# Kernel optimization log

Hardware: AMD Instinct MI355X
Metric: run time of the kernel (lower is better)

The kernel has to match this reference:

```python
import jax, jax.numpy as jnp
import numpy as np

B, L, D, H = 256, 256, 128, 256
IMPUTE_WEIGHT = 1.0


def setup_inputs() -> dict:
    key = jax.random.key(0)
    ks = jax.random.split(key, 20)
    s = 0.05
    inp = {
        "values": jax.random.normal(ks[0], (B, L, D), jnp.float32),
        "masks": jax.random.randint(ks[1], (B, L, D), 0, 2).astype(jnp.float32),
        "deltas": jax.random.uniform(ks[2], (B, L, D), jnp.float32),
        "eval_masks": jax.random.randint(ks[3], (B, L, D), 0, 2).astype(jnp.float32),
        "td_h_W": jax.random.normal(ks[4], (H, D), jnp.float32) * s,
        "td_h_b": jax.random.normal(ks[5], (H,), jnp.float32) * s,
        "td_x_w": jax.random.normal(ks[6], (D,), jnp.float32) * s,  # diag of TemporalDecay(diag=True)
        "td_x_b": jax.random.normal(ks[7], (D,), jnp.float32) * s,
        "hist_W": jax.random.normal(ks[8], (D, H), jnp.float32) * s,
        "hist_b": jax.random.normal(ks[9], (D,), jnp.float32) * s,
        "feat_W": jax.random.normal(ks[10], (D, D), jnp.float32) * s,
        "feat_b": jax.random.normal(ks[11], (D,), jnp.float32) * s,
        "wc_W": jax.random.normal(ks[12], (D, 2 * D), jnp.float32) * s,
        "wc_b": jax.random.normal(ks[13], (D,), jnp.float32) * s,
        "W_ih": jax.random.normal(ks[14], (4 * H, 2 * D), jnp.float32) * s,
        "W_hh": jax.random.normal(ks[15], (4 * H, H), jnp.float32) * s,
        "b_ih": jax.random.normal(ks[16], (4 * H,), jnp.float32) * s,
        "b_hh": jax.random.normal(ks[17], (4 * H,), jnp.float32) * s,
    }
    return inp


def _rits_forward(values, masks, deltas, eval_masks,
                  td_h_W, td_h_b, td_x_w, td_x_b,
                  hist_W, hist_b, feat_W, feat_b,
                  wc_W, wc_b, W_ih, W_hh, b_ih, b_hh):
    feat_mask = 1.0 - jnp.eye(D, dtype=values.dtype)  # zero diagonal
    Wf = feat_W * feat_mask

    def step(carry, xs):
        h, c, loss = carry
        x, m, d, me = xs  # each (B, D)
        gamma_h = jnp.exp(-jax.nn.relu(d @ td_h_W.T + td_h_b))   # (B, H)
        gamma_x = jnp.exp(-jax.nn.relu(d * td_x_w + td_x_b))      # (B, D) diag linear
        h = h * gamma_h
        x_h = h @ hist_W.T + hist_b                               # (B, D)
        x_c = m * x + (1.0 - m) * x_h
        z_h = x_c @ Wf.T + feat_b                                 # (B, D)
        alpha = jnp.concatenate([gamma_x, m], axis=1) @ wc_W.T + wc_b
        c_h = alpha * z_h + (1.0 - alpha) * x_h
        c_c = m * x + (1.0 - m) * c_h
        loss = loss + jnp.sum(jnp.abs(c_c - x) * me) / (jnp.sum(me) + 1e-5)
        inputs = jnp.concatenate([c_c, m], axis=1)                # (B, 2D)
        gates = inputs @ W_ih.T + b_ih + h @ W_hh.T + b_hh        # (B, 4H)
        i, f, g, o = jnp.split(gates, 4, axis=1)
        i, f, o = jax.nn.sigmoid(i), jax.nn.sigmoid(f), jax.nn.sigmoid(o)
        g = jnp.tanh(g)
        c = f * c + i * g
        h = o * jnp.tanh(c)
        return (h, c, loss), c_c

    h0 = jnp.zeros((values.shape[0], H), values.dtype)
    c0 = jnp.zeros((values.shape[0], H), values.dtype)
    loss0 = jnp.zeros((), values.dtype)
    xs = (jnp.swapaxes(values, 0, 1), jnp.swapaxes(masks, 0, 1),
          jnp.swapaxes(deltas, 0, 1), jnp.swapaxes(eval_masks, 0, 1))  # (L, B, D)
    (_, _, loss), imps = jax.lax.scan(step, (h0, c0, loss0), xs)
    imputations = jnp.swapaxes(imps, 0, 1)  # (B, L, D)
    return imputations, loss * IMPUTE_WEIGHT


def reference(values, masks, deltas, eval_masks,
              td_h_W, td_h_b, td_x_w, td_x_b,
              hist_W, hist_b, feat_W, feat_b,
              wc_W, wc_b, W_ih, W_hh, b_ih, b_hh):
    return _rits_forward(values, masks, deltas, eval_masks,
                         td_h_W, td_h_b, td_x_w, td_x_b,
                         hist_W, hist_b, feat_W, feat_b,
                         wc_W, wc_b, W_ih, W_hh, b_ih, b_hh)
```

## Files before the change

kernel.cpp:

```cpp
#include <hip/hip_runtime.h>
#include <math.h>


namespace {
constexpr int Bn = 256, Ln = 256, Dn = 128, Hn = 256;
constexpr long LD = (long)Ln * Dn;

constexpr int OFF_LOSS  = 0;
constexpr int OFF_DEN   = 256;
constexpr int OFF_BIASG = 2048;
constexpr int OFF_WG    = 8192;
constexpr int OFF_HISTP = 1056768;
constexpr int OFF_TDHP  = 1122304;
constexpr int OFF_WFP   = 1187840;
constexpr int OFF_WCP   = 1220608;
constexpr int OFF_EXCH  = 1310720;
constexpr int OFF_FLAG  = 2097152;
}

typedef _Float16 h2f __attribute__((ext_vector_type(2)));
typedef unsigned int uint32;
typedef unsigned long long uint64;

__device__ __forceinline__ float fdot2(uint32 a, uint32 b, float c) {
  return __builtin_amdgcn_fdot2(__builtin_bit_cast(h2f, a),
                                __builtin_bit_cast(h2f, b), c, false);
}
__device__ __forceinline__ uint32 packf16(float a, float b) {
  h2f p; p[0] = (_Float16)a; p[1] = (_Float16)b;
  return __builtin_bit_cast(uint32, p);
}
__device__ __forceinline__ unsigned short f16u(float a) {
  _Float16 h = (_Float16)a; return __builtin_bit_cast(unsigned short, h);
}

__global__ void rits_prep(const float* __restrict__ td_h_W,
                          const float* __restrict__ hist_W,
                          const float* __restrict__ feat_W,
                          const float* __restrict__ wc_W,
                          const float* __restrict__ W_ih,
                          const float* __restrict__ W_hh,
                          const float* __restrict__ b_ih,
                          const float* __restrict__ b_hh,
                          const float* __restrict__ evalm,
                          char* __restrict__ wsb) {
  const int blk = blockIdx.x, tid = threadIdx.x;
  if (blk < 1248) {
    int idx = blk * 256 + tid;
    if (idx < 262144) {
      int kp = idx >> 11, rem = idx & 2047, jj = rem >> 3, s8 = rem & 7;
      const float* src = (s8 < 4) ? W_ih : W_hh;
      int q = s8 & 3;
      const float* row = src + (size_t)(q * 256 + jj) * 256 + 2 * kp;
      ((uint32*)(wsb + OFF_WG))[idx] = packf16(row[0], row[1]);
    } else if (idx < 278528) {
      int i2 = idx - 262144, kp = i2 >> 7, d = i2 & 127;
      ((uint32*)(wsb + OFF_HISTP))[i2] =
          packf16(hist_W[d * 256 + 2 * kp], hist_W[d * 256 + 2 * kp + 1]);
    } else if (idx < 294912) {
      int i2 = idx - 278528, kp = i2 >> 8, h = i2 & 255;
      ((uint32*)(wsb + OFF_TDHP))[i2] =
          packf16(td_h_W[h * 128 + 2 * kp], td_h_W[h * 128 + 2 * kp + 1]);
    } else if (idx < 303104) {
      int i2 = idx - 294912, kp = i2 >> 7, d = i2 & 127;
      float a = (2 * kp == d) ? 0.f : feat_W[d * 128 + 2 * kp];
      float b = (2 * kp + 1 == d) ? 0.f : feat_W[d * 128 + 2 * kp + 1];
      ((uint32*)(wsb + OFF_WFP))[i2] = packf16(a, b);
    } else if (idx < 319488) {
      int i2 = idx - 303104, kp = i2 >> 7, d = i2 & 127;
      ((uint32*)(wsb + OFF_WCP))[i2] =
          packf16(wc_W[d * 256 + 2 * kp], wc_W[d * 256 + 2 * kp + 1]);
    }
  } else if (blk < 1252) {
    int i = (blk - 1248) * 256 + tid;
    int jj = i >> 2, q = i & 3;
    ((float*)(wsb + OFF_BIASG))[jj * 4 + q] =
        b_ih[q * 256 + jj] + b_hh[q * 256 + jj];
    if (blk == 1248 && tid == 0) *((float*)(wsb + OFF_LOSS)) = 0.f;
  } else if (blk < 1508) {
    int t = blk - 1252;
    __shared__ float red[256];
    int d = tid & 127, g = tid >> 7;
    float s = 0.f;
    for (int b = g; b < 256; b += 2) s += evalm[(size_t)b * LD + t * 128 + d];
    red[tid] = s;
    __syncthreads();
    for (int o = 128; o > 0; o >>= 1) {
      if (tid < o) red[tid] += red[tid + o];
      __syncthreads();
    }
    if (tid == 0) ((float*)(wsb + OFF_DEN))[t] = red[0] + 1e-5f;
  } else {
    for (int i = tid; i < 4096; i += 256) ((uint32*)(wsb + OFF_FLAG))[i] = 0u;
  }
}

__global__ __launch_bounds__(1024, 4) void rits_rec(
    const float* __restrict__ values, const float* __restrict__ masks,
    const float* __restrict__ deltas, const float* __restrict__ evalm,
    const float* __restrict__ td_h_b, const float* __restrict__ td_x_w,
    const float* __restrict__ td_x_b, const float* __restrict__ hist_b,
    const float* __restrict__ feat_b, const float* __restrict__ wc_b,
    char* __restrict__ wsb, float* __restrict__ outp) {
  __shared__ __align__(16) float scratch[8448];
  __shared__ float den_s[256], bg_s[512], tdhb_s[128];
  __shared__ float txw_s[128], txb_s[128], hb_s[128], fb_s[128], wcb_s[128];
  __shared__ float hf[2][128], cst[2][128];
  __shared__ float xs[2][128], ms[2][128], es[2][128];
  __shared__ float xhp[2][2][128];
  __shared__ float xh_s[2][128], al_s[2][128];
  __shared__ __align__(8) unsigned short hdU16[128 * 4];
  __shared__ __align__(8) unsigned short cmU16[128 * 4];
  __shared__ __align__(8) unsigned short xcU16[64 * 4];
  __shared__ uint32 drP[64 * 2];
  __shared__ uint32 gxmP[128 * 2];

  const int tid = threadIdx.x;
  const int bid = blockIdx.x;
  const int sh = bid >> 7;
  const int pair = bid & 127;
  const size_t b0 = (size_t)pair * 2;
  const uint32* hdU32 = (const uint32*)hdU16;
  const uint32* cmU32 = (const uint32*)cmU16;
  const uint32* xcU32 = (const uint32*)xcU16;
  const uint32* wg = (const uint32*)(wsb + OFF_WG);
  const uint4* histP4 = (const uint4*)(wsb + OFF_HISTP);
  const uint4* tdhP4 = (const uint4*)(wsb + OFF_TDHP);
  const uint4* wfP4 = (const uint4*)(wsb + OFF_WFP);
  const uint4* wcP4 = (const uint4*)(wsb + OFF_WCP);
  char* exch = wsb + OFF_EXCH;
  unsigned int* myf = (unsigned int*)(wsb + OFF_FLAG + ((pair << 1) | sh) * 64);
  unsigned int* pf  = (unsigned int*)(wsb + OFF_FLAG + ((pair << 1) | (sh ^ 1)) * 64);

  if (tid < 512) bg_s[tid] = ((const float*)(wsb + OFF_BIASG))[sh * 512 + tid];
  else if (tid < 768) den_s[tid - 512] = ((const float*)(wsb + OFF_DEN))[tid - 512];
  else if (tid < 896) tdhb_s[tid - 768] = td_h_b[(sh << 7) + (tid - 768)];
  else txw_s[tid - 896] = td_x_w[tid - 896];
  if (tid < 128) txb_s[tid] = td_x_b[tid];
  else if (tid < 256) hb_s[tid - 128] = hist_b[tid - 128];
  else if (tid < 384) fb_s[tid - 256] = feat_b[tid - 256];
  else if (tid < 512) wcb_s[tid - 384] = wc_b[tid - 384];
  else {
    int i = tid - 512;
    if (i < 256) ((float*)hf)[i] = 0.f;
    else ((float*)cst)[i - 256] = 0.f;
  }
  __syncthreads();

  float lacc = 0.f;
  for (int t = 0; t < Ln; ++t) {
    const size_t base = b0 * LD + (size_t)t * 128;
    uint64* myp = (uint64*)(exch + ((((pair << 1) | sh) << 1) | (t & 1)) * 1536);
    uint64* pp  = (uint64*)(exch + ((((pair << 1) | (sh ^ 1)) << 1) | (t & 1)) * 1536);

    if (tid < 256) {
      int d = tid & 127, r = tid >> 7;
      size_t gi = base + (size_t)r * LD + d;
      xs[r][d] = values[gi];
      ms[r][d] = masks[gi];
      es[r][d] = evalm[gi];
    } else if (tid < 512) {
      int i = tid - 256, kp = i & 127, r = i >> 7;
      size_t gb = base + (size_t)r * LD;
      if (kp < 64) {
        float d0v = deltas[gb + 2 * kp], d1v = deltas[gb + 2 * kp + 1];
        drP[kp * 2 + r] = packf16(d0v, d1v);
        float g0 = __expf(-fmaxf(fmaf(d0v, txw_s[2 * kp], txb_s[2 * kp]), 0.f));
        float g1 = __expf(-fmaxf(fmaf(d1v, txw_s[2 * kp + 1], txb_s[2 * kp + 1]), 0.f));
        gxmP[kp * 2 + r] = packf16(g0, g1);
      } else {
        int k2 = kp - 64;
        gxmP[kp * 2 + r] = packf16(masks[gb + 2 * k2], masks[gb + 2 * k2 + 1]);
      }
    }
    __syncthreads();

    if (tid < 256) {
      int g = tid & 31, r = (tid >> 5) & 1, kq = tid >> 6;
      int gg = (sh << 5) + g;
      float4 a = {0.f, 0.f, 0.f, 0.f};
#pragma unroll 4
      for (int i = 0; i < 16; ++i) {
        int kp = kq * 16 + i;
        uint4 w = tdhP4[kp * 64 + gg];
        uint32 dr = drP[kp * 2 + r];
        a.x = fdot2(dr, w.x, a.x); a.y = fdot2(dr, w.y, a.y);
        a.z = fdot2(dr, w.z, a.z); a.w = fdot2(dr, w.w, a.w);
      }
      ((float4*)(scratch + (kq * 2 + r) * 132))[g] = a;
    } else if (tid < 768) {
      int i0 = tid - 256, g = i0 & 31, r = (i0 >> 5) & 1, kq = i0 >> 6;
      float4 a = {0.f, 0.f, 0.f, 0.f};
#pragma unroll 4
      for (int i = 0; i < 16; ++i) {
        int kp = kq * 16 + i;
        uint4 w = wcP4[kp * 32 + g];
        uint32 gm = gxmP[kp * 2 + r];
        a.x = fdot2(gm, w.x, a.x); a.y = fdot2(gm, w.y, a.y);
        a.z = fdot2(gm, w.z, a.z); a.w = fdot2(gm, w.w, a.w);
      }
      ((float4*)(scratch + 1056 + (kq * 2 + r) * 132))[g] = a;
    }
    __syncthreads();

    if (tid < 256) {
      int hl = tid & 127, r = tid >> 7;
      float ssum = tdhb_s[hl];
#pragma unroll
      for (int kq = 0; kq < 4; ++kq) ssum += scratch[(kq * 2 + r) * 132 + hl];
      float hd = hf[r][hl] * __expf(-fmaxf(ssum, 0.f));
      int hg = (sh << 7) | hl;
      hdU16[(hg >> 1) * 4 + 2 * r + (hg & 1)] = f16u(hd);
    } else if (tid >= 512 && tid < 768) {
      int i0 = tid - 512, d = i0 & 127, r = i0 >> 7;
      float ssum = wcb_s[d];
#pragma unroll
      for (int kq = 0; kq < 8; ++kq) ssum += scratch[1056 + (kq * 2 + r) * 132 + d];
      al_s[r][d] = ssum;
    }
    __syncthreads();

    if (tid < 512) {
      int g = tid & 31, r = (tid >> 5) & 1, kq = tid >> 6;
      float4 a = {0.f, 0.f, 0.f, 0.f};
#pragma unroll 4
      for (int i = 0; i < 8; ++i) {
        int kp = (sh << 6) + kq * 8 + i;
        uint4 w = histP4[kp * 32 + g];
        uint32 hd = hdU32[kp * 2 + r];
        a.x = fdot2(hd, w.x, a.x); a.y = fdot2(hd, w.y, a.y);
        a.z = fdot2(hd, w.z, a.z); a.w = fdot2(hd, w.w, a.w);
      }
      ((float4*)(scratch + (kq * 2 + r) * 132))[g] = a;
    } else if (tid < 576) {
      int i = tid - 512;
      uint64 v = ((const uint64*)hdU16)[(sh << 6) + i];
      __hip_atomic_store(myp + i, v, __ATOMIC_RELAXED, __HIP_MEMORY_SCOPE_AGENT);
    }
    __syncthreads();

    if (tid < 256) {
      int d = tid & 127, r = tid >> 7;
      float xo = 0.f;
#pragma unroll
      for (int kq = 0; kq < 8; ++kq) xo += scratch[(kq * 2 + r) * 132 + d];
      xhp[sh][r][d] = xo;
      __hip_atomic_store((uint32*)myp + 128 + (r << 7) + d,
                         __builtin_bit_cast(uint32, xo),
                         __ATOMIC_RELAXED, __HIP_MEMORY_SCOPE_AGENT);
    }
    __syncthreads();

    if (tid == 0) {
      __hip_atomic_store(myf, (unsigned)(t + 1), __ATOMIC_RELEASE,
                         __HIP_MEMORY_SCOPE_AGENT);
      unsigned guard = 0;
      while (__hip_atomic_load(pf, __ATOMIC_ACQUIRE,
                               __HIP_MEMORY_SCOPE_AGENT) < (unsigned)(t + 1)) {
        if (++guard > (1u << 22)) break;
      }
    }
    __syncthreads();

    if (tid < 192) {
      uint64 v = __hip_atomic_load(pp + tid, __ATOMIC_RELAXED,
                                   __HIP_MEMORY_SCOPE_AGENT);
      if (tid < 64) {
        ((uint64*)hdU16)[((sh ^ 1) << 6) + tid] = v;
      } else {
        int j = tid - 64;
        int r = j >> 6, d2 = (j & 63) << 1;
        xhp[sh ^ 1][r][d2] = __builtin_bit_cast(float, (uint32)v);
        xhp[sh ^ 1][r][d2 + 1] = __builtin_bit_cast(float, (uint32)(v >> 32));
      }
    }
    __syncthreads();

    if (tid < 256) {
      int d = tid & 127, r = tid >> 7;
      float xh = xhp[0][r][d] + xhp[1][r][d] + hb_s[d];
      xh_s[r][d] = xh;
      float mm = ms[r][d];
      float xc = mm * xs[r][d] + (1.f - mm) * xh;
      xcU16[(d >> 1) * 4 + 2 * r + (d & 1)] = f16u(xc);
    }
    __syncthreads();

    if (tid < 512) {
      int g = tid & 31, r = (tid >> 5) & 1, kq = tid >> 6;
      float4 a = {0.f, 0.f, 0.f, 0.f};
#pragma unroll 4
      for (int i = 0; i < 8; ++i) {
        int kp = kq * 8 + i;
        uint4 w = wfP4[kp * 32 + g];
        uint32 xc = xcU32[kp * 2 + r];
        a.x = fdot2(xc, w.x, a.x); a.y = fdot2(xc, w.y, a.y);
        a.z = fdot2(xc, w.z, a.z); a.w = fdot2(xc, w.w, a.w);
      }
      ((float4*)(scratch + (kq * 2 + r) * 132))[g] = a;
    }
    __syncthreads();

    if (tid < 256) {
      int d = tid & 127, r = tid >> 7;
      float z = fb_s[d];
#pragma unroll
      for (int kq = 0; kq < 8; ++kq) z += scratch[(kq * 2 + r) * 132 + d];
      float a = al_s[r][d], xh = xh_s[r][d];
      float ch = a * z + (1.f - a) * xh;
      float mm = ms[r][d], xv = xs[r][d];
      float cc = mm * xv + (1.f - mm) * ch;
      if (r == sh) {
        outp[base + (size_t)r * LD + d] = cc;
        lacc += (1.f - mm) * fabsf(ch - xv) * es[r][d] / den_s[t];
      }
      cmU16[(d >> 1) * 4 + 2 * r + (d & 1)] = f16u(cc);
      cmU16[(64 + (d >> 1)) * 4 + 2 * r + (d & 1)] = f16u(mm);
    }
    __syncthreads();

    {
      int jj = tid & 127, kq = tid >> 7;
      int jg = (sh << 7) | jj;
      int kp0 = kq * 16;
      const uint4* wp = (const uint4*)(wg + ((size_t)kp0 * 256 + jg) * 8);
      float a00 = 0, a01 = 0, a02 = 0, a03 = 0;
      float a10 = 0, a11 = 0, a12 = 0, a13 = 0;
#pragma unroll 4
      for (int i = 0; i < 16; ++i) {
        int kp = kp0 + i;
        uint4 wv = wp[0];
        uint4 wh = wp[1];
        wp += 512;
        uint32 c0 = cmU32[kp * 2 + 0], c1 = cmU32[kp * 2 + 1];
        uint32 h0 = hdU32[kp * 2 + 0], h1 = hdU32[kp * 2 + 1];
        a00 = fdot2(c0, wv.x, a00); a01 = fdot2(c0, wv.y, a01);
        a02 = fdot2(c0, wv.z, a02); a03 = fdot2(c0, wv.w, a03);
        a10 = fdot2(c1, wv.x, a10); a11 = fdot2(c1, wv.y, a11);
        a12 = fdot2(c1, wv.z, a12); a13 = fdot2(c1, wv.w, a13);
        a00 = fdot2(h0, wh.x, a00); a01 = fdot2(h0, wh.y, a01);
        a02 = fdot2(h0, wh.z, a02); a03 = fdot2(h0, wh.w, a03);
        a10 = fdot2(h1, wh.x, a10); a11 = fdot2(h1, wh.y, a11);
        a12 = fdot2(h1, wh.z, a12); a13 = fdot2(h1, wh.w, a13);
      }
      float* pg = scratch;
      pg[(kq * 8 + 0) * 132 + jj] = a00; pg[(kq * 8 + 1) * 132 + jj] = a01;
      pg[(kq * 8 + 2) * 132 + jj] = a02; pg[(kq * 8 + 3) * 132 + jj] = a03;
      pg[(kq * 8 + 4) * 132 + jj] = a10; pg[(kq * 8 + 5) * 132 + jj] = a11;
      pg[(kq * 8 + 6) * 132 + jj] = a12; pg[(kq * 8 + 7) * 132 + jj] = a13;
    }
    __syncthreads();

    if (tid < 256) {
      int jj = tid & 127, r = tid >> 7;
      float g0 = bg_s[jj * 4 + 0], g1 = bg_s[jj * 4 + 1];
      float g2 = bg_s[jj * 4 + 2], g3 = bg_s[jj * 4 + 3];
#pragma unroll
      for (int kq = 0; kq < 8; ++kq) {
        int bix = (kq * 8 + r * 4) * 132 + jj;
        g0 += scratch[bix]; g1 += scratch[bix + 132];
        g2 += scratch[bix + 264]; g3 += scratch[bix + 396];
      }
      float ig = 1.f / (1.f + __expf(-g0));
      float fg = 1.f / (1.f + __expf(-g1));
      float gg = tanhf(g2);
      float og = 1.f / (1.f + __expf(-g3));
      float c = fg * cst[r][jj] + ig * gg;
      cst[r][jj] = c;
      hf[r][jj] = og * tanhf(c);
    }
    __syncthreads();
  }

  scratch[tid] = lacc;
  __syncthreads();
  for (int o = 512; o > 0; o >>= 1) {
    if (tid < o) scratch[tid] += scratch[tid + o];
    __syncthreads();
  }
  if (tid == 0) atomicAdd((float*)(wsb + OFF_LOSS), scratch[0]);
}

__global__ void rits_fin(const char* __restrict__ wsb, float* __restrict__ outp) {
  if (threadIdx.x == 0 && blockIdx.x == 0)
    outp[(size_t)Bn * LD] = *((const float*)(wsb + OFF_LOSS));
}

extern "C" void kernel_launch(void* const* d_in, const int* in_sizes, int n_in,
                              void* d_out, int out_size, void* d_ws,
                              size_t ws_size, hipStream_t stream) {
  const float* values = (const float*)d_in[0];
  const float* masks  = (const float*)d_in[1];
  const float* deltas = (const float*)d_in[2];
  const float* evalm  = (const float*)d_in[3];
  const float* td_h_W = (const float*)d_in[4];
  const float* td_h_b = (const float*)d_in[5];
  const float* td_x_w = (const float*)d_in[6];
  const float* td_x_b = (const float*)d_in[7];
  const float* hist_W = (const float*)d_in[8];
  const float* hist_b = (const float*)d_in[9];
  const float* feat_W = (const float*)d_in[10];
  const float* feat_b = (const float*)d_in[11];
  const float* wc_W   = (const float*)d_in[12];
  const float* wc_b   = (const float*)d_in[13];
  const float* W_ih   = (const float*)d_in[14];
  const float* W_hh   = (const float*)d_in[15];
  const float* b_ih   = (const float*)d_in[16];
  const float* b_hh   = (const float*)d_in[17];
  char* wsb = (char*)d_ws;
  float* outp = (float*)d_out;

  hipLaunchKernelGGL(rits_prep, dim3(1509), dim3(256), 0, stream, td_h_W,
                     hist_W, feat_W, wc_W, W_ih, W_hh, b_ih, b_hh, evalm, wsb);
  hipLaunchKernelGGL(rits_rec, dim3(256), dim3(1024), 0, stream, values, masks,
                     deltas, evalm, td_h_b, td_x_w, td_x_b, hist_b, feat_b,
                     wc_b, wsb, outp);
  hipLaunchKernelGGL(rits_fin, dim3(1), dim3(64), 0, stream, wsb, outp);
}
```

Baseline: 3.563 ms.

## Split recurrence across four cooperating blocks per four-sample group

Restructures the recurrent kernel so each workgroup of four blocks handles four batch rows, with each block owning a quarter of the hidden units and gate outputs, instead of pairs of blocks owning two rows. Each block now exchanges partial h, alpha and history projections with three peers through global memory flags, and the weight-column slices it streams per step are halved. The intent is to cut per-step weight traffic per sample and raise arithmetic reuse of each loaded weight. The cost is more cross-block synchronisation per step, with three peer waits instead of one.

```diff
diff --git a/kernel.cpp b/kernel.cpp
--- a/kernel.cpp
+++ b/kernel.cpp
@@ -14,13 +14,12 @@
 constexpr int OFF_TDHP  = 1122304;
 constexpr int OFF_WFP   = 1187840;
 constexpr int OFF_WCP   = 1220608;
-constexpr int OFF_EXCH  = 1310720;
-constexpr int OFF_FLAG  = 2097152;
+constexpr int OFF_EXCH  = 1286144;
+constexpr int OFF_FLAG  = 2859008;
 }
 
 typedef _Float16 h2f __attribute__((ext_vector_type(2)));
 typedef unsigned int uint32;
-typedef unsigned long long uint64;
 
 __device__ __forceinline__ float fdot2(uint32 a, uint32 b, float c) {
   return __builtin_amdgcn_fdot2(__builtin_bit_cast(h2f, a),
@@ -102,210 +101,238 @@
     const float* __restrict__ td_x_b, const float* __restrict__ hist_b,
     const float* __restrict__ feat_b, const float* __restrict__ wc_b,
     char* __restrict__ wsb, float* __restrict__ outp) {
-  __shared__ __align__(16) float scratch[8448];
-  __shared__ float den_s[256], bg_s[512], tdhb_s[128];
+  __shared__ __align__(16) float scratch[16384];
+  __shared__ float den_s[256], bg_s[256], tdhb_s[64];
   __shared__ float txw_s[128], txb_s[128], hb_s[128], fb_s[128], wcb_s[128];
-  __shared__ float hf[2][128], cst[2][128];
-  __shared__ float xs[2][128], ms[2][128], es[2][128];
-  __shared__ float xhp[2][2][128];
-  __shared__ float xh_s[2][128], al_s[2][128];
-  __shared__ __align__(8) unsigned short hdU16[128 * 4];
-  __shared__ __align__(8) unsigned short cmU16[128 * 4];
-  __shared__ __align__(8) unsigned short xcU16[64 * 4];
-  __shared__ uint32 drP[64 * 2];
-  __shared__ uint32 gxmP[128 * 2];
+  __shared__ float hf[4][64], cst[4][64];
+  __shared__ float xs[4][128], ms[4][128], es[4][128];
+  __shared__ float xhp[4][4][128];
+  __shared__ float xh_s[4][128], al_s[4][128];
+  __shared__ uint32 hdP[128 * 4];
+  __shared__ uint32 cmP[128 * 4];
+  __shared__ uint32 xcP[64 * 4];
+  __shared__ uint32 drP[64 * 4];
+  __shared__ uint32 gxmP[128 * 4];
 
   const int tid = threadIdx.x;
   const int bid = blockIdx.x;
-  const int sh = bid >> 7;
-  const int pair = bid & 127;
-  const size_t b0 = (size_t)pair * 2;
-  const uint32* hdU32 = (const uint32*)hdU16;
-  const uint32* cmU32 = (const uint32*)cmU16;
-  const uint32* xcU32 = (const uint32*)xcU16;
+  const int sh = bid >> 6;
+  const int grp = bid & 63;
+  const size_t b0 = (size_t)grp * 4;
   const uint32* wg = (const uint32*)(wsb + OFF_WG);
   const uint4* histP4 = (const uint4*)(wsb + OFF_HISTP);
   const uint4* tdhP4 = (const uint4*)(wsb + OFF_TDHP);
   const uint4* wfP4 = (const uint4*)(wsb + OFF_WFP);
   const uint4* wcP4 = (const uint4*)(wsb + OFF_WCP);
   char* exch = wsb + OFF_EXCH;
-  unsigned int* myf = (unsigned int*)(wsb + OFF_FLAG + ((pair << 1) | sh) * 64);
-  unsigned int* pf  = (unsigned int*)(wsb + OFF_FLAG + ((pair << 1) | (sh ^ 1)) * 64);
-
-  if (tid < 512) bg_s[tid] = ((const float*)(wsb + OFF_BIASG))[sh * 512 + tid];
-  else if (tid < 768) den_s[tid - 512] = ((const float*)(wsb + OFF_DEN))[tid - 512];
-  else if (tid < 896) tdhb_s[tid - 768] = td_h_b[(sh << 7) + (tid - 768)];
-  else txw_s[tid - 896] = td_x_w[tid - 896];
-  if (tid < 128) txb_s[tid] = td_x_b[tid];
-  else if (tid < 256) hb_s[tid - 128] = hist_b[tid - 128];
-  else if (tid < 384) fb_s[tid - 256] = feat_b[tid - 256];
-  else if (tid < 512) wcb_s[tid - 384] = wc_b[tid - 384];
-  else {
-    int i = tid - 512;
-    if (i < 256) ((float*)hf)[i] = 0.f;
-    else ((float*)cst)[i - 256] = 0.f;
-  }
+  unsigned int* flg = (unsigned int*)(wsb + OFF_FLAG);
+
+  if (tid < 256) bg_s[tid] = ((const float*)(wsb + OFF_BIASG))[sh * 256 + tid];
+  else if (tid < 512) den_s[tid - 256] = ((const float*)(wsb + OFF_DEN))[tid - 256];
+  else if (tid < 576) tdhb_s[tid - 512] = td_h_b[sh * 64 + (tid - 512)];
+  else if (tid < 704) txw_s[tid - 576] = td_x_w[tid - 576];
+  else if (tid < 832) txb_s[tid - 704] = td_x_b[tid - 704];
+  else if (tid < 960) hb_s[tid - 832] = hist_b[tid - 832];
+  if (tid < 128) fb_s[tid] = feat_b[tid];
+  else if (tid < 256) wcb_s[tid - 128] = wc_b[tid - 128];
+  else if (tid < 512) ((float*)hf)[tid - 256] = 0.f;
+  else if (tid < 768) ((float*)cst)[tid - 512] = 0.f;
   __syncthreads();
 
   float lacc = 0.f;
   for (int t = 0; t < Ln; ++t) {
     const size_t base = b0 * LD + (size_t)t * 128;
-    uint64* myp = (uint64*)(exch + ((((pair << 1) | sh) << 1) | (t & 1)) * 1536);
-    uint64* pp  = (uint64*)(exch + ((((pair << 1) | (sh ^ 1)) << 1) | (t & 1)) * 1536);
-
-    if (tid < 256) {
+    uint32* mypU = (uint32*)(exch + (size_t)(bid * 2 + (t & 1)) * 3072);
+
+    if (tid < 512) {
       int d = tid & 127, r = tid >> 7;
       size_t gi = base + (size_t)r * LD + d;
       xs[r][d] = values[gi];
       ms[r][d] = masks[gi];
       es[r][d] = evalm[gi];
-    } else if (tid < 512) {
-      int i = tid - 256, kp = i & 127, r = i >> 7;
+    } else {
+      int i = tid - 512, kp = i & 127, r = i >> 7;
       size_t gb = base + (size_t)r * LD;
       if (kp < 64) {
         float d0v = deltas[gb + 2 * kp], d1v = deltas[gb + 2 * kp + 1];
-        drP[kp * 2 + r] = packf16(d0v, d1v);
+        drP[kp * 4 + r] = packf16(d0v, d1v);
         float g0 = __expf(-fmaxf(fmaf(d0v, txw_s[2 * kp], txb_s[2 * kp]), 0.f));
         float g1 = __expf(-fmaxf(fmaf(d1v, txw_s[2 * kp + 1], txb_s[2 * kp + 1]), 0.f));
-        gxmP[kp * 2 + r] = packf16(g0, g1);
+        gxmP[kp * 4 + r] = packf16(g0, g1);
       } else {
         int k2 = kp - 64;
-        gxmP[kp * 2 + r] = packf16(masks[gb + 2 * k2], masks[gb + 2 * k2 + 1]);
-      }
-    }
-    __syncthreads();
-
-    if (tid < 256) {
-      int g = tid & 31, r = (tid >> 5) & 1, kq = tid >> 6;
-      int gg = (sh << 5) + g;
-      float4 a = {0.f, 0.f, 0.f, 0.f};
-#pragma unroll 4
-      for (int i = 0; i < 16; ++i) {
-        int kp = kq * 16 + i;
-        uint4 w = tdhP4[kp * 64 + gg];
-        uint32 dr = drP[kp * 2 + r];
-        a.x = fdot2(dr, w.x, a.x); a.y = fdot2(dr, w.y, a.y);
-        a.z = fdot2(dr, w.z, a.z); a.w = fdot2(dr, w.w, a.w);
-      }
-      ((float4*)(scratch + (kq * 2 + r) * 132))[g] = a;
-    } else if (tid < 768) {
-      int i0 = tid - 256, g = i0 & 31, r = (i0 >> 5) & 1, kq = i0 >> 6;
-      float4 a = {0.f, 0.f, 0.f, 0.f};
-#pragma unroll 4
-      for (int i = 0; i < 16; ++i) {
-        int kp = kq * 16 + i;
-        uint4 w = wcP4[kp * 32 + g];
-        uint32 gm = gxmP[kp * 2 + r];
-        a.x = fdot2(gm, w.x, a.x); a.y = fdot2(gm, w.y, a.y);
-        a.z = fdot2(gm, w.z, a.z); a.w = fdot2(gm, w.w, a.w);
-      }
-      ((float4*)(scratch + 1056 + (kq * 2 + r) * 132))[g] = a;
-    }
-    __syncthreads();
-
-    if (tid < 256) {
-      int hl = tid & 127, r = tid >> 7;
-      float ssum = tdhb_s[hl];
-#pragma unroll
-      for (int kq = 0; kq < 4; ++kq) ssum += scratch[(kq * 2 + r) * 132 + hl];
-      float hd = hf[r][hl] * __expf(-fmaxf(ssum, 0.f));
-      int hg = (sh << 7) | hl;
-      hdU16[(hg >> 1) * 4 + 2 * r + (hg & 1)] = f16u(hd);
-    } else if (tid >= 512 && tid < 768) {
-      int i0 = tid - 512, d = i0 & 127, r = i0 >> 7;
-      float ssum = wcb_s[d];
-#pragma unroll
-      for (int kq = 0; kq < 8; ++kq) ssum += scratch[1056 + (kq * 2 + r) * 132 + d];
-      al_s[r][d] = ssum;
-    }
-    __syncthreads();
-
-    if (tid < 512) {
-      int g = tid & 31, r = (tid >> 5) & 1, kq = tid >> 6;
-      float4 a = {0.f, 0.f, 0.f, 0.f};
+        gxmP[kp * 4 + r] = packf16(masks[gb + 2 * k2], masks[gb + 2 * k2 + 1]);
+      }
+    }
+    __syncthreads();
+
+    if (tid < 128) {
+      int g = tid & 15, kq = tid >> 4;
+      int kp0 = kq * 8;
+      float4 a0 = {0,0,0,0}, a1 = a0, a2 = a0, a3 = a0;
 #pragma unroll 4
       for (int i = 0; i < 8; ++i) {
-        int kp = (sh << 6) + kq * 8 + i;
+        int kp = kp0 + i;
+        uint4 w = tdhP4[kp * 64 + sh * 16 + g];
+        uint32 d0 = drP[kp*4+0], d1 = drP[kp*4+1], d2 = drP[kp*4+2], d3 = drP[kp*4+3];
+        a0.x = fdot2(d0,w.x,a0.x); a0.y = fdot2(d0,w.y,a0.y); a0.z = fdot2(d0,w.z,a0.z); a0.w = fdot2(d0,w.w,a0.w);
+        a1.x = fdot2(d1,w.x,a1.x); a1.y = fdot2(d1,w.y,a1.y); a1.z = fdot2(d1,w.z,a1.z); a1.w = fdot2(d1,w.w,a1.w);
+        a2.x = fdot2(d2,w.x,a2.x); a2.y = fdot2(d2,w.y,a2.y); a2.z = fdot2(d2,w.z,a2.z); a2.w = fdot2(d2,w.w,a2.w);
+        a3.x = fdot2(d3,w.x,a3.x); a3.y = fdot2(d3,w.y,a3.y); a3.z = fdot2(d3,w.z,a3.z); a3.w = fdot2(d3,w.w,a3.w);
+      }
+      ((float4*)scratch)[(kq*4+0)*17 + g] = a0;
+      ((float4*)scratch)[(kq*4+1)*17 + g] = a1;
+      ((float4*)scratch)[(kq*4+2)*17 + g] = a2;
+      ((float4*)scratch)[(kq*4+3)*17 + g] = a3;
+    } else if (tid < 256) {
+      int i0 = tid - 128, g = i0 & 7, kq = i0 >> 3;
+      int kp0 = kq * 8;
+      float4 a0 = {0,0,0,0}, a1 = a0, a2 = a0, a3 = a0;
+#pragma unroll 4
+      for (int i = 0; i < 8; ++i) {
+        int kp = kp0 + i;
+        uint4 w = wcP4[kp * 32 + sh * 8 + g];
+        uint32 g0 = gxmP[kp*4+0], g1 = gxmP[kp*4+1], g2 = gxmP[kp*4+2], g3 = gxmP[kp*4+3];
+        a0.x = fdot2(g0,w.x,a0.x); a0.y = fdot2(g0,w.y,a0.y); a0.z = fdot2(g0,w.z,a0.z); a0.w = fdot2(g0,w.w,a0.w);
+        a1.x = fdot2(g1,w.x,a1.x); a1.y = fdot2(g1,w.y,a1.y); a1.z = fdot2(g1,w.z,a1.z); a1.w = fdot2(g1,w.w,a1.w);
+        a2.x = fdot2(g2,w.x,a2.x); a2.y = fdot2(g2,w.y,a2.y); a2.z = fdot2(g2,w.z,a2.z); a2.w = fdot2(g2,w.w,a2.w);
+        a3.x = fdot2(g3,w.x,a3.x); a3.y = fdot2(g3,w.y,a3.y); a3.z = fdot2(g3,w.z,a3.z); a3.w = fdot2(g3,w.w,a3.w);
+      }
+      ((float4*)(scratch + 2304))[(kq*4+0)*9 + g] = a0;
+      ((float4*)(scratch + 2304))[(kq*4+1)*9 + g] = a1;
+      ((float4*)(scratch + 2304))[(kq*4+2)*9 + g] = a2;
+      ((float4*)(scratch + 2304))[(kq*4+3)*9 + g] = a3;
+    }
+    __syncthreads();
+
+    if (tid < 256) {
+      int hl = tid & 63, r = tid >> 6;
+      float ssum = tdhb_s[hl];
+#pragma unroll
+      for (int kq = 0; kq < 8; ++kq) ssum += scratch[(kq*4+r)*68 + hl];
+      float hd = hf[r][hl] * __expf(-fmaxf(ssum, 0.f));
+      int h = sh * 64 + hl, kp = h >> 1;
+      ((unsigned short*)hdP)[(kp*4+r)*2 + (h & 1)] = f16u(hd);
+    } else if (tid < 384) {
+      int i0 = tid - 256, dl = i0 & 31, r = i0 >> 5;
+      float ssum = wcb_s[sh*32 + dl];
+#pragma unroll
+      for (int kq = 0; kq < 16; ++kq) ssum += scratch[2304 + (kq*4+r)*36 + dl];
+      al_s[r][sh*32 + dl] = ssum;
+      __hip_atomic_store(mypU + 128 + r*32 + dl, __builtin_bit_cast(uint32, ssum),
+                         __ATOMIC_RELAXED, __HIP_MEMORY_SCOPE_AGENT);
+    }
+    __syncthreads();
+
+    if (tid < 512) {
+      int g = tid & 31, kq = tid >> 5;
+      int kp0 = sh * 32 + kq * 2;
+      float4 a0 = {0,0,0,0}, a1 = a0, a2 = a0, a3 = a0;
+#pragma unroll
+      for (int i = 0; i < 2; ++i) {
+        int kp = kp0 + i;
         uint4 w = histP4[kp * 32 + g];
-        uint32 hd = hdU32[kp * 2 + r];
-        a.x = fdot2(hd, w.x, a.x); a.y = fdot2(hd, w.y, a.y);
-        a.z = fdot2(hd, w.z, a.z); a.w = fdot2(hd, w.w, a.w);
-      }
-      ((float4*)(scratch + (kq * 2 + r) * 132))[g] = a;
-    } else if (tid < 576) {
-      int i = tid - 512;
-      uint64 v = ((const uint64*)hdU16)[(sh << 6) + i];
-      __hip_atomic_store(myp + i, v, __ATOMIC_RELAXED, __HIP_MEMORY_SCOPE_AGENT);
-    }
-    __syncthreads();
-
-    if (tid < 256) {
+        uint32 h0 = hdP[kp*4+0], h1 = hdP[kp*4+1], h2 = hdP[kp*4+2], h3 = hdP[kp*4+3];
+        a0.x = fdot2(h0,w.x,a0.x); a0.y = fdot2(h0,w.y,a0.y); a0.z = fdot2(h0,w.z,a0.z); a0.w = fdot2(h0,w.w,a0.w);
+        a1.x = fdot2(h1,w.x,a1.x); a1.y = fdot2(h1,w.y,a1.y); a1.z = fdot2(h1,w.z,a1.z); a1.w = fdot2(h1,w.w,a1.w);
+        a2.x = fdot2(h2,w.x,a2.x); a2.y = fdot2(h2,w.y,a2.y); a2.z = fdot2(h2,w.z,a2.z); a2.w = fdot2(h2,w.w,a2.w);
+        a3.x = fdot2(h3,w.x,a3.x); a3.y = fdot2(h3,w.y,a3.y); a3.z = fdot2(h3,w.z,a3.z); a3.w = fdot2(h3,w.w,a3.w);
+      }
+      ((float4*)scratch)[(kq*4+0)*33 + g] = a0;
+      ((float4*)scratch)[(kq*4+1)*33 + g] = a1;
+      ((float4*)scratch)[(kq*4+2)*33 + g] = a2;
+      ((float4*)scratch)[(kq*4+3)*33 + g] = a3;
+    } else if (tid < 640) {
+      int i0 = tid - 512, kpl = i0 >> 2, r = i0 & 3;
+      uint32 v = hdP[(sh*32 + kpl)*4 + r];
+      __hip_atomic_store(mypU + kpl*4 + r, v, __ATOMIC_RELAXED,
+                         __HIP_MEMORY_SCOPE_AGENT);
+    }
+    __syncthreads();
+
+    if (tid < 512) {
       int d = tid & 127, r = tid >> 7;
       float xo = 0.f;
 #pragma unroll
-      for (int kq = 0; kq < 8; ++kq) xo += scratch[(kq * 2 + r) * 132 + d];
+      for (int kq = 0; kq < 16; ++kq) xo += scratch[(kq*4+r)*132 + d];
       xhp[sh][r][d] = xo;
-      __hip_atomic_store((uint32*)myp + 128 + (r << 7) + d,
-                         __builtin_bit_cast(uint32, xo),
+      __hip_atomic_store(mypU + 256 + r*128 + d, __builtin_bit_cast(uint32, xo),
                          __ATOMIC_RELAXED, __HIP_MEMORY_SCOPE_AGENT);
     }
     __syncthreads();
 
-    if (tid == 0) {
-      __hip_atomic_store(myf, (unsigned)(t + 1), __ATOMIC_RELEASE,
+    if (tid == 0)
+      __hip_atomic_store(flg + bid * 16, (unsigned)(t + 1), __ATOMIC_RELEASE,
                          __HIP_MEMORY_SCOPE_AGENT);
+    if (tid < 3) {
+      int ps = tid + (tid >= sh ? 1 : 0);
+      unsigned* pfp = flg + (ps * 64 + grp) * 16;
       unsigned guard = 0;
-      while (__hip_atomic_load(pf, __ATOMIC_ACQUIRE,
+      while (__hip_atomic_load(pfp, __ATOMIC_ACQUIRE,
                                __HIP_MEMORY_SCOPE_AGENT) < (unsigned)(t + 1)) {
         if (++guard > (1u << 22)) break;
       }
     }
     __syncthreads();
 
-    if (tid < 192) {
-      uint64 v = __hip_atomic_load(pp + tid, __ATOMIC_RELAXED,
-                                   __HIP_MEMORY_SCOPE_AGENT);
-      if (tid < 64) {
-        ((uint64*)hdU16)[((sh ^ 1) << 6) + tid] = v;
+    if (tid < 768) {
+      int p = tid >> 8, j = tid & 255;
+      int ps = p + (p >= sh ? 1 : 0);
+      const uint32* pq =
+          (const uint32*)(exch + (size_t)((ps * 64 + grp) * 2 + (t & 1)) * 3072);
+      uint32 v0 = __hip_atomic_load(pq + j, __ATOMIC_RELAXED, __HIP_MEMORY_SCOPE_AGENT);
+      uint32 v1 = __hip_atomic_load(pq + 256 + j, __ATOMIC_RELAXED, __HIP_MEMORY_SCOPE_AGENT);
+      uint32 v2 = __hip_atomic_load(pq + 512 + j, __ATOMIC_RELAXED, __HIP_MEMORY_SCOPE_AGENT);
+      if (j < 128) {
+        int kpl = j >> 2, r = j & 3;
+        hdP[(ps*32 + kpl)*4 + r] = v0;
       } else {
-        int j = tid - 64;
-        int r = j >> 6, d2 = (j & 63) << 1;
-        xhp[sh ^ 1][r][d2] = __builtin_bit_cast(float, (uint32)v);
-        xhp[sh ^ 1][r][d2 + 1] = __builtin_bit_cast(float, (uint32)(v >> 32));
-      }
-    }
-    __syncthreads();
-
-    if (tid < 256) {
+        int i = j - 128, r = i >> 5, dl = i & 31;
+        al_s[r][ps*32 + dl] = __builtin_bit_cast(float, v0);
+      }
+      int r1 = j >> 7, d1 = j & 127;
+      xhp[ps][r1][d1] = __builtin_bit_cast(float, v1);
+      xhp[ps][2 + r1][d1] = __builtin_bit_cast(float, v2);
+    }
+    __syncthreads();
+
+    if (tid < 512) {
       int d = tid & 127, r = tid >> 7;
-      float xh = xhp[0][r][d] + xhp[1][r][d] + hb_s[d];
+      float xh = ((xhp[0][r][d] + xhp[1][r][d]) + (xhp[2][r][d] + xhp[3][r][d]))
+                 + hb_s[d];
       xh_s[r][d] = xh;
       float mm = ms[r][d];
       float xc = mm * xs[r][d] + (1.f - mm) * xh;
-      xcU16[(d >> 1) * 4 + 2 * r + (d & 1)] = f16u(xc);
-    }
-    __syncthreads();
-
-    if (tid < 512) {
-      int g = tid & 31, r = (tid >> 5) & 1, kq = tid >> 6;
-      float4 a = {0.f, 0.f, 0.f, 0.f};
-#pragma unroll 4
-      for (int i = 0; i < 8; ++i) {
-        int kp = kq * 8 + i;
+      ((unsigned short*)xcP)[((d >> 1)*4 + r)*2 + (d & 1)] = f16u(xc);
+    }
+    __syncthreads();
+
+    if (tid < 512) {
+      int g = tid & 31, kq = tid >> 5;
+      int kp0 = kq * 4;
+      float4 a0 = {0,0,0,0}, a1 = a0, a2 = a0, a3 = a0;
+#pragma unroll
+      for (int i = 0; i < 4; ++i) {
+        int kp = kp0 + i;
         uint4 w = wfP4[kp * 32 + g];
-        uint32 xc = xcU32[kp * 2 + r];
-        a.x = fdot2(xc, w.x, a.x); a.y = fdot2(xc, w.y, a.y);
-        a.z = fdot2(xc, w.z, a.z); a.w = fdot2(xc, w.w, a.w);
-      }
-      ((float4*)(scratch + (kq * 2 + r) * 132))[g] = a;
-    }
-    __syncthreads();
-
-    if (tid < 256) {
+        uint32 x0 = xcP[kp*4+0], x1 = xcP[kp*4+1], x2 = xcP[kp*4+2], x3 = xcP[kp*4+3];
+        a0.x = fdot2(x0,w.x,a0.x); a0.y = fdot2(x0,w.y,a0.y); a0.z = fdot2(x0,w.z,a0.z); a0.w = fdot2(x0,w.w,a0.w);
+        a1.x = fdot2(x1,w.x,a1.x); a1.y = fdot2(x1,w.y,a1.y); a1.z = fdot2(x1,w.z,a1.z); a1.w = fdot2(x1,w.w,a1.w);
+        a2.x = fdot2(x2,w.x,a2.x); a2.y = fdot2(x2,w.y,a2.y); a2.z = fdot2(x2,w.z,a2.z); a2.w = fdot2(x2,w.w,a2.w);
+        a3.x = fdot2(x3,w.x,a3.x); a3.y = fdot2(x3,w.y,a3.y); a3.z = fdot2(x3,w.z,a3.z); a3.w = fdot2(x3,w.w,a3.w);
+      }
+      ((float4*)scratch)[(kq*4+0)*33 + g] = a0;
+      ((float4*)scratch)[(kq*4+1)*33 + g] = a1;
+      ((float4*)scratch)[(kq*4+2)*33 + g] = a2;
+      ((float4*)scratch)[(kq*4+3)*33 + g] = a3;
+    }
+    __syncthreads();
+
+    if (tid < 512) {
       int d = tid & 127, r = tid >> 7;
       float z = fb_s[d];
 #pragma unroll
-      for (int kq = 0; kq < 8; ++kq) z += scratch[(kq * 2 + r) * 132 + d];
+      for (int kq = 0; kq < 16; ++kq) z += scratch[(kq*4+r)*132 + d];
       float a = al_s[r][d], xh = xh_s[r][d];
       float ch = a * z + (1.f - a) * xh;
       float mm = ms[r][d], xv = xs[r][d];
@@ -314,52 +341,48 @@
         outp[base + (size_t)r * LD + d] = cc;
         lacc += (1.f - mm) * fabsf(ch - xv) * es[r][d] / den_s[t];
       }
-      cmU16[(d >> 1) * 4 + 2 * r + (d & 1)] = f16u(cc);
-      cmU16[(64 + (d >> 1)) * 4 + 2 * r + (d & 1)] = f16u(mm);
+      ((unsigned short*)cmP)[((d >> 1)*4 + r)*2 + (d & 1)] = f16u(cc);
+      ((unsigned short*)cmP)[((64 + (d >> 1))*4 + r)*2 + (d & 1)] = f16u(mm);
     }
     __syncthreads();
 
     {
-      int jj = tid & 127, kq = tid >> 7;
-      int jg = (sh << 7) | jj;
-      int kp0 = kq * 16;
+      int jj = tid & 63, kq = tid >> 6;
+      int jg = sh * 64 + jj, kp0 = kq * 8;
       const uint4* wp = (const uint4*)(wg + ((size_t)kp0 * 256 + jg) * 8);
-      float a00 = 0, a01 = 0, a02 = 0, a03 = 0;
-      float a10 = 0, a11 = 0, a12 = 0, a13 = 0;
+      float a[4][4] = {};
 #pragma unroll 4
-      for (int i = 0; i < 16; ++i) {
+      for (int i = 0; i < 8; ++i) {
         int kp = kp0 + i;
         uint4 wv = wp[0];
         uint4 wh = wp[1];
         wp += 512;
-        uint32 c0 = cmU32[kp * 2 + 0], c1 = cmU32[kp * 2 + 1];
-        uint32 h0 = hdU32[kp * 2 + 0], h1 = hdU32[kp * 2 + 1];
-        a00 = fdot2(c0, wv.x, a00); a01 = fdot2(c0, wv.y, a01);
-        a02 = fdot2(c0, wv.z, a02); a03 = fdot2(c0, wv.w, a03);
-        a10 = fdot2(c1, wv.x, a10); a11 = fdot2(c1, wv.y, a11);
-        a12 = fdot2(c1, wv.z, a12); a13 = fdot2(c1, wv.w, a13);
-        a00 = fdot2(h0, wh.x, a00); a01 = fdot2(h0, wh.y, a01);
-        a02 = fdot2(h0, wh.z, a02); a03 = fdot2(h0, wh.w, a03);
-        a10 = fdot2(h1, wh.x, a10); a11 = fdot2(h1, wh.y, a11);
-        a12 = fdot2(h1, wh.z, a12); a13 = fdot2(h1, wh.w, a13);
-      }
-      float* pg = scratch;
-      pg[(kq * 8 + 0) * 132 + jj] = a00; pg[(kq * 8 + 1) * 132 + jj] = a01;
-      pg[(kq * 8 + 2) * 132 + jj] = a02; pg[(kq * 8 + 3) * 132 + jj] = a03;
-      pg[(kq * 8 + 4) * 132 + jj] = a10; pg[(kq * 8 + 5) * 132 + jj] = a11;
-      pg[(kq * 8 + 6) * 132 + jj] = a12; pg[(kq * 8 + 7) * 132 + jj] = a13;
+#pragma unroll
+        for (int r = 0; r < 4; ++r) {
+          uint32 c = cmP[kp*4 + r], h = hdP[kp*4 + r];
+          a[r][0] = fdot2(c, wv.x, a[r][0]); a[r][1] = fdot2(c, wv.y, a[r][1]);
+          a[r][2] = fdot2(c, wv.z, a[r][2]); a[r][3] = fdot2(c, wv.w, a[r][3]);
+          a[r][0] = fdot2(h, wh.x, a[r][0]); a[r][1] = fdot2(h, wh.y, a[r][1]);
+          a[r][2] = fdot2(h, wh.z, a[r][2]); a[r][3] = fdot2(h, wh.w, a[r][3]);
+        }
+      }
+#pragma unroll
+      for (int r = 0; r < 4; ++r)
+#pragma unroll
+        for (int q = 0; q < 4; ++q)
+          scratch[(kq*16 + r*4 + q)*64 + jj] = a[r][q];
     }
     __syncthreads();
 
     if (tid < 256) {
-      int jj = tid & 127, r = tid >> 7;
-      float g0 = bg_s[jj * 4 + 0], g1 = bg_s[jj * 4 + 1];
-      float g2 = bg_s[jj * 4 + 2], g3 = bg_s[jj * 4 + 3];
-#pragma unroll
-      for (int kq = 0; kq < 8; ++kq) {
-        int bix = (kq * 8 + r * 4) * 132 + jj;
-        g0 += scratch[bix]; g1 += scratch[bix + 132];
-        g2 += scratch[bix + 264]; g3 += scratch[bix + 396];
+      int jj = tid & 63, r = tid >> 6;
+      float g0 = bg_s[jj*4+0], g1 = bg_s[jj*4+1];
+      float g2 = bg_s[jj*4+2], g3 = bg_s[jj*4+3];
+#pragma unroll
+      for (int kq = 0; kq < 16; ++kq) {
+        int bix = (kq*16 + r*4)*64 + jj;
+        g0 += scratch[bix]; g1 += scratch[bix + 64];
+        g2 += scratch[bix + 128]; g3 += scratch[bix + 192];
       }
       float ig = 1.f / (1.f + __expf(-g0));
       float fg = 1.f / (1.f + __expf(-g1));
```

Result: slower. 4.814 ms (+35.1%).
